# Kernel optimization log

Hardware: AMD Instinct MI355X
Metric: run time of the kernel (lower is better)

Reference implementation:

```python
import jax, jax.numpy as jnp
from jax import lax
import numpy as np

IMG_CH = 3
C = 48            # total channels
HIDDEN = 256
FIRE_RATE = 0.5
DX_NOISE = 0.0
NEG_SLOPE = 0.01  # torch LeakyReLU default


def _dwconv(x_nchw, w):
    # depthwise 3x3 conv with reflect padding, w: [C,1,3,3]
    xp = jnp.pad(x_nchw, ((0, 0), (0, 0), (1, 1), (1, 1)), mode='reflect')
    return lax.conv_general_dilated(
        xp, w, window_strides=(1, 1), padding='VALID',
        feature_group_count=C,
        dimension_numbers=('NCHW', 'OIHW', 'NCHW'))


def setup_inputs() -> dict:
    key = jax.random.key(0)
    ks = jax.random.split(key, 6)
    x = jax.random.normal(ks[0], (8, 256, 256, C), dtype=jnp.float32)
    filt0 = jax.random.normal(ks[1], (C, 1, 3, 3), dtype=jnp.float32) * 0.1
    filt1 = jax.random.normal(ks[2], (C, 1, 3, 3), dtype=jnp.float32) * 0.1
    fan_in = 3 * C
    w1 = jax.random.normal(ks[3], (HIDDEN, 3 * C), dtype=jnp.float32) / np.sqrt(fan_in).astype(np.float32)
    b1 = jax.random.normal(ks[4], (HIDDEN,), dtype=jnp.float32) * 0.01
    # original zero-inits w2; randomized small so outputs/grads are nontrivial
    w2 = jax.random.normal(ks[5], (C, HIDDEN), dtype=jnp.float32) * 0.02
    return {"x": x, "filt0": filt0, "filt1": filt1, "w1": w1, "b1": b1, "w2": w2, "steps": 4}


def reference(x, filt0, filt1, w1, b1, w2, steps):
    ch_mask = (jnp.arange(C) >= IMG_CH).astype(x.dtype)  # immutable image channels
    rng = jax.random.key(42)
    for i in range(steps):
        xc = jnp.transpose(x, (0, 3, 1, 2))                       # [B,C,H,W]
        p = jnp.concatenate([xc, _dwconv(xc, filt0), _dwconv(xc, filt1)], axis=1)
        p = jnp.transpose(p, (0, 2, 3, 1))                        # [B,H,W,3C]
        h = jax.nn.leaky_relu(jnp.einsum('bhwf,of->bhwo', p, w1) + b1, NEG_SLOPE)
        d = jnp.einsum('bhwo,co->bhwc', h, w2)                    # [B,H,W,C]
        k1, k2 = jax.random.split(jax.random.fold_in(rng, i))
        fire = (jax.random.uniform(k1, d.shape[:3] + (1,)) > FIRE_RATE).astype(d.dtype)
        d = d * fire + DX_NOISE * jax.random.normal(k2, d.shape[:3] + (1,), dtype=d.dtype)
        d = d * ch_mask
        x = x + d
    return x
```

## Files before the change

### kernel.cpp

```cpp
#include <hip/hip_runtime.h>
#include <stdint.h>
#include <stddef.h>


#define B_   8
#define H_   256
#define W_   256
#define C_   48
#define F_   144
#define HID_ 256
#define PW_  64
#define NTOT (B_*H_*W_*C_)
#define XSTR 56

typedef __attribute__((ext_vector_type(8))) short short8;
typedef __attribute__((ext_vector_type(4))) float f32x4;

struct U2 { unsigned x, y; };

__host__ __device__ __forceinline__ unsigned rotl32(unsigned v, int r) {
  return (v << r) | (v >> (32 - r));
}

__host__ __device__ __forceinline__ U2 threefry2x32(unsigned k0, unsigned k1,
                                                    unsigned x0, unsigned x1) {
  const unsigned k2 = k0 ^ k1 ^ 0x1BD11BDAu;
  x0 += k0; x1 += k1;
#define TF_R(r) { x0 += x1; x1 = rotl32(x1, r); x1 ^= x0; }
  TF_R(13) TF_R(15) TF_R(26) TF_R(6)
  x0 += k1; x1 += k2 + 1u;
  TF_R(17) TF_R(29) TF_R(16) TF_R(24)
  x0 += k2; x1 += k0 + 2u;
  TF_R(13) TF_R(15) TF_R(26) TF_R(6)
  x0 += k0; x1 += k1 + 3u;
  TF_R(17) TF_R(29) TF_R(16) TF_R(24)
  x0 += k1; x1 += k2 + 4u;
  TF_R(13) TF_R(15) TF_R(26) TF_R(6)
  x0 += k2; x1 += k0 + 5u;
#undef TF_R
  U2 r; r.x = x0; r.y = x1; return r;
}

__device__ __forceinline__ unsigned short f2bf(float f) {
  unsigned u = __float_as_uint(f);
  unsigned r = u + 0x7FFFu + ((u >> 16) & 1u);
  return (unsigned short)(r >> 16);
}
__device__ __forceinline__ unsigned packbf2(float lo, float hi) {
  return (unsigned)f2bf(lo) | ((unsigned)f2bf(hi) << 16);
}
__device__ __forceinline__ float bf2f(unsigned short u) {
  return __uint_as_float(((unsigned)u) << 16);
}

#define W1B_N 114688
#define W2B_N 12288
__global__ void nca_pack(const float* __restrict__ w1,
                         const float* __restrict__ w2,
                         const float* __restrict__ f0,
                         const float* __restrict__ f1,
                         unsigned short* __restrict__ w1B,
                         unsigned short* __restrict__ w2B) {
  int i = blockIdx.x * 256 + threadIdx.x;
  if (i < W1B_N) {
    int ntg = i / 7168, r = i - ntg * 7168;
    int ks = r >> 9, r2 = r & 511;
    int lane = r2 >> 3, j = r2 & 7;
    int o = ntg * 16 + (lane & 15);
    int k = ks * 32 + (lane >> 4) * 8 + j;
    float v = 0.0f;
    if (k < 432) {
      int tap = k / 48, c = k - tap * 48;
      v = w1[o * F_ + 48 + c] * f0[c * 9 + tap]
        + w1[o * F_ + 96 + c] * f1[c * 9 + tap];
      if (tap == 4) v += w1[o * F_ + c];
    }
    w1B[i] = f2bf(v);
  }
  if (i < W2B_N) {
    int nt = i >> 12, r = i & 4095;
    int ks = r >> 9, r2 = r & 511;
    int lane = r2 >> 3, j = r2 & 7;
    int c = nt * 16 + (lane & 15);
    int o = ks * 32 + (lane >> 4) * 8 + j;
    w2B[i] = f2bf(w2[c * HID_ + o]);
  }
}

template<int INBF, int OUTBF>
__global__ __launch_bounds__(256, 3)
void nca_step(const void* __restrict__ xin_, void* __restrict__ xout_,
              const unsigned short* __restrict__ w1B,
              const float* __restrict__ b1,
              const unsigned short* __restrict__ w2Bp,
              unsigned ka, unsigned kb) {
  __shared__ __align__(16) char smem[32768];
  __shared__ float fireL[PW_];
  short* xT = (short*)smem;
  short* hA = (short*)smem;

  const int t = threadIdx.x;
  const int bid = blockIdx.x;
  const int wseg = bid & 3;
  const int h = (bid >> 2) & 255;
  const int b = bid >> 10;
  const int w0 = wseg * PW_;
  const int gbase = ((b * H_ + h) * W_ + w0) * C_;

  if (t < PW_) {
    unsigned j = (unsigned)((b * H_ + h) * W_ + w0 + t);
    U2 r = threefry2x32(ka, kb, 0u, j);
    unsigned bits = r.x ^ r.y;
    fireL[t] = ((bits >> 9) > 4194304u) ? 1.0f : 0.0f;
  }
  {
    const int hr[3] = { (h == 0) ? 1 : h - 1, h, (h == 255) ? 254 : h + 1 };
#pragma unroll
    for (int g = 0; g < 10; ++g) {
      int i = t + g * 256;
      if (i < 2376) {
        int row = i / 792, rem = i - row * 792;
        int px = rem / 12, c4 = rem - px * 12;
        int w = w0 - 1 + px;
        int wg = (w < 0) ? 1 : (w > 255) ? 254 : w;
        const int gidx = ((b * H_ + hr[row]) * W_ + wg) * C_ + c4 * 4;
        uint2 d;
        if constexpr (INBF) {
          d = *(const uint2*)((const unsigned short*)xin_ + gidx);
        } else {
          const float4 v = *(const float4*)((const float*)xin_ + gidx);
          d.x = packbf2(v.x, v.y); d.y = packbf2(v.z, v.w);
        }
        *(uint2*)&xT[(row * 66 + px) * XSTR + c4 * 4] = d;
      }
    }
  }
  __syncthreads();

  const int wv = t >> 6, lane = t & 63;
  const int c16 = lane & 15, quad = lane >> 4;
  f32x4 acc[4][4];
#pragma unroll
  for (int mt = 0; mt < 4; ++mt)
#pragma unroll
    for (int nt = 0; nt < 4; ++nt) acc[mt][nt] = f32x4{0.f, 0.f, 0.f, 0.f};

#define LDA1(dst, ksl) { int ch_ = (ksl) * 4 + quad; \
  if ((ksl) == 13 && ch_ > 53) ch_ = 53;  \
  const int tap_ = ch_ / 6;    \
  const int o_ = ((tap_ / 3) * 66 + c16 + (tap_ - (tap_ / 3) * 3)) * XSTR \
                 + (ch_ - tap_ * 6) * 8; \
  _Pragma("unroll") for (int mt = 0; mt < 4; ++mt) \
    dst[mt] = *(const short8*)&xT[o_ + mt * (16 * XSTR)]; }
#define LDB1(dst, ksl) { _Pragma("unroll") for (int nt = 0; nt < 4; ++nt) \
  dst[nt] = *(const short8*)&w1B[((((wv * 4 + nt) * 14 + (ksl)) << 6) | lane) << 3]; }
#define MM1(aa, bb) { _Pragma("unroll") for (int nt = 0; nt < 4; ++nt) \
  _Pragma("unroll") for (int mt = 0; mt < 4; ++mt) \
    acc[mt][nt] = __builtin_amdgcn_mfma_f32_16x16x32_bf16(aa[mt], bb[nt], acc[mt][nt], 0, 0, 0); }

  {
    short8 aP[4], aQ[4], bX[4], bY[4], bZ[4];
    LDB1(bX, 0) LDB1(bY, 1) LDA1(aP, 0)
    LDA1(aQ, 1)  LDB1(bZ, 2)   MM1(aP, bX)
    LDA1(aP, 2)  LDB1(bX, 3)   MM1(aQ, bY)
    LDA1(aQ, 3)  LDB1(bY, 4)   MM1(aP, bZ)
    LDA1(aP, 4)  LDB1(bZ, 5)   MM1(aQ, bX)
    LDA1(aQ, 5)  LDB1(bX, 6)   MM1(aP, bY)
    LDA1(aP, 6)  LDB1(bY, 7)   MM1(aQ, bZ)
    LDA1(aQ, 7)  LDB1(bZ, 8)   MM1(aP, bX)
    LDA1(aP, 8)  LDB1(bX, 9)   MM1(aQ, bY)
    LDA1(aQ, 9)  LDB1(bY, 10)  MM1(aP, bZ)
    LDA1(aP, 10) LDB1(bZ, 11)  MM1(aQ, bX)
    LDA1(aQ, 11) LDB1(bX, 12)  MM1(aP, bY)
    LDA1(aP, 12) LDB1(bY, 13)  MM1(aQ, bZ)
    LDA1(aQ, 13)               MM1(aP, bX)
                               MM1(aQ, bY)
  }
#undef LDA1
#undef LDB1
#undef MM1

#define LDW2(dst, ksl) { _Pragma("unroll") for (int nt = 0; nt < 3; ++nt) \
  dst[nt] = *(const short8*)&w2Bp[((((nt) * 8 + (ksl)) << 6) | lane) << 3]; }
#define LDH2(dst, ksl) dst = *(const short8*)&hA[(((wv * 8 + (ksl)) << 6) | lane) << 3];
#define MM2(hh, ww) { _Pragma("unroll") for (int nt = 0; nt < 3; ++nt) \
  acc2[nt] = __builtin_amdgcn_mfma_f32_16x16x32_bf16(hh, ww[nt], acc2[nt], 0, 0, 0); }

  short8 wA[3], wB[3], wC[3];
  LDW2(wA, 0) LDW2(wB, 1)

  unsigned short bs[3][4];
  if constexpr (INBF) {
#pragma unroll
    for (int nt = 0; nt < 3; ++nt)
#pragma unroll
      for (int reg = 0; reg < 4; ++reg)
        bs[nt][reg] = (unsigned short)
          xT[(66 + 1 + wv * 16 + quad * 4 + reg) * XSTR + nt * 16 + c16];
  }
  __syncthreads();

#pragma unroll
  for (int nt = 0; nt < 4; ++nt) {
    const int o = (wv * 4 + nt) * 16 + c16;
    const float bias = b1[o];
    const int ks2 = o >> 5, q2 = (o & 31) >> 3, j2 = o & 7;
#pragma unroll
    for (int mt = 0; mt < 4; ++mt) {
#pragma unroll
      for (int reg = 0; reg < 4; ++reg) {
        float z = acc[mt][nt][reg] + bias;
        z = (z >= 0.f) ? z : 0.01f * z;
        const int lane2 = (quad * 4 + reg) + (q2 << 4);
        hA[((((mt * 8 + ks2) << 6) | lane2) << 3) + j2] = (short)f2bf(z);
      }
    }
  }
  __syncthreads();

  {
    f32x4 acc2[3];
#pragma unroll
    for (int nt = 0; nt < 3; ++nt) acc2[nt] = f32x4{0.f, 0.f, 0.f, 0.f};

    short8 h0, h1;
    LDH2(h0, 0)
    LDH2(h1, 1) LDW2(wC, 2) MM2(h0, wA)
    LDH2(h0, 2) LDW2(wA, 3) MM2(h1, wB)
    LDH2(h1, 3) LDW2(wB, 4) MM2(h0, wC)
    LDH2(h0, 4) LDW2(wC, 5) MM2(h1, wA)
    LDH2(h1, 5) LDW2(wA, 6) MM2(h0, wB)
    LDH2(h0, 6) LDW2(wB, 7) MM2(h1, wC)
    LDH2(h1, 7)             MM2(h0, wA)
                            MM2(h1, wB)

#pragma unroll
    for (int nt = 0; nt < 3; ++nt) {
      const int c = nt * 16 + c16;
#pragma unroll
      for (int reg = 0; reg < 4; ++reg) {
        const int pxl = wv * 16 + quad * 4 + reg;
        float d = acc2[nt][reg] * fireL[pxl];
        if (c < 3) d = 0.f;
        const int idx = gbase + pxl * C_ + c;
        float base;
        if constexpr (INBF) base = bf2f(bs[nt][reg]);
        else                base = ((const float*)xin_)[idx];
        const float r = base + d;
        if constexpr (OUTBF) ((unsigned short*)xout_)[idx] = f2bf(r);
        else                 ((float*)xout_)[idx] = r;
      }
    }
  }
#undef LDW2
#undef LDH2
#undef MM2
}

extern "C" void kernel_launch(void* const* d_in, const int* in_sizes, int n_in,
                              void* d_out, int out_size, void* d_ws, size_t ws_size,
                              hipStream_t stream) {
  const float* xin = (const float*)d_in[0];
  const float* f0  = (const float*)d_in[1];
  const float* f1  = (const float*)d_in[2];
  const float* w1  = (const float*)d_in[3];
  const float* b1  = (const float*)d_in[4];
  const float* w2  = (const float*)d_in[5];
  float* xout = (float*)d_out;
  (void)in_sizes; (void)n_in; (void)out_size; (void)ws_size;

  unsigned ka[4], kb[4];
  for (int i = 0; i < 4; ++i) {
    U2 fold = threefry2x32(0u, 42u, 0u, (unsigned)i);
    U2 k1 = threefry2x32(fold.x, fold.y, 0u, 0u);
    ka[i] = k1.x; kb[i] = k1.y;
  }

  unsigned short* w1B = (unsigned short*)d_ws;
  unsigned short* w2B = w1B + W1B_N;
  unsigned short* xb  = (unsigned short*)((char*)d_ws + (size_t)(W1B_N + W2B_N) * 2);
  unsigned short* ob  = (unsigned short*)d_out;

  const dim3 gs(B_ * H_ * (W_ / PW_));
  const dim3 bs(256);

  nca_pack<<<(W1B_N + 255) / 256, 256, 0, stream>>>(w1, w2, f0, f1, w1B, w2B);
  nca_step<0, 1><<<gs, bs, 0, stream>>>(xin, xb,   w1B, b1, w2B, ka[0], kb[0]);
  nca_step<1, 1><<<gs, bs, 0, stream>>>(xb,  ob,   w1B, b1, w2B, ka[1], kb[1]);
  nca_step<1, 1><<<gs, bs, 0, stream>>>(ob,  xb,   w1B, b1, w2B, ka[2], kb[2]);
  nca_step<1, 0><<<gs, bs, 0, stream>>>(xb,  xout, w1B, b1, w2B, ka[3], kb[3]);
}
```

Baseline: 821.6 us.

## Use direct global-to-LDS loads, swap MFMA operands, and pack bf16 conversions

For bf16 inputs, the interior of the halo tile is now loaded straight into LDS with global_load_lds, and the LDS row stride drops from 56 to 48 to match the contiguous layout. Only the edge pixels still go through registers. The w1 packing order changes to k-slice-major, and the MFMA operands are swapped so the accumulator holds output channels along the register dimension. That lets the bias be read as a float4 and the hidden activations stored as packed bf16 pairs using v_cvt_pk_bf16_f32, and the K loop is rewritten as a double-buffered loop. The narrower stride risks LDS bank conflicts, and the hardware rounding may differ slightly from the old software rounding.

```diff
diff --git a/kernel.cpp b/kernel.cpp
--- a/kernel.cpp
+++ b/kernel.cpp
@@ -11,10 +11,16 @@
 #define HID_ 256
 #define PW_  64
 #define NTOT (B_*H_*W_*C_)
-#define XSTR 56
+#define XSTR 48
 
 typedef __attribute__((ext_vector_type(8))) short short8;
 typedef __attribute__((ext_vector_type(4))) float f32x4;
+
+typedef const __attribute__((address_space(1))) char* gas_t;
+typedef __attribute__((address_space(3))) char* las_t;
+__device__ __forceinline__ void gload16(const char* g, char* l) {
+  __builtin_amdgcn_global_load_lds((gas_t)g, (las_t)l, 16, 0, 0);
+}
 
 struct U2 { unsigned x, y; };
 
@@ -41,13 +47,15 @@
   U2 r; r.x = x0; r.y = x1; return r;
 }
 
-__device__ __forceinline__ unsigned short f2bf(float f) {
+__host__ __device__ __forceinline__ unsigned short f2bf(float f) {
   unsigned u = __float_as_uint(f);
   unsigned r = u + 0x7FFFu + ((u >> 16) & 1u);
   return (unsigned short)(r >> 16);
 }
 __device__ __forceinline__ unsigned packbf2(float lo, float hi) {
-  return (unsigned)f2bf(lo) | ((unsigned)f2bf(hi) << 16);
+  unsigned r;
+  asm("v_cvt_pk_bf16_f32 %0, %1, %2" : "=v"(r) : "v"(lo), "v"(hi));
+  return r;
 }
 __device__ __forceinline__ float bf2f(unsigned short u) {
   return __uint_as_float(((unsigned)u) << 16);
@@ -63,8 +71,8 @@
                          unsigned short* __restrict__ w2B) {
   int i = blockIdx.x * 256 + threadIdx.x;
   if (i < W1B_N) {
-    int ntg = i / 7168, r = i - ntg * 7168;
-    int ks = r >> 9, r2 = r & 511;
+    int ks = i >> 13, r = i & 8191;
+    int ntg = r >> 9, r2 = r & 511;
     int lane = r2 >> 3, j = r2 & 7;
     int o = ntg * 16 + (lane & 15);
     int k = ks * 32 + (lane >> 4) * 8 + j;
@@ -115,23 +123,38 @@
   }
   {
     const int hr[3] = { (h == 0) ? 1 : h - 1, h, (h == 255) ? 254 : h + 1 };
-#pragma unroll
-    for (int g = 0; g < 10; ++g) {
-      int i = t + g * 256;
-      if (i < 2376) {
-        int row = i / 792, rem = i - row * 792;
-        int px = rem / 12, c4 = rem - px * 12;
+    if constexpr (INBF) {
+#pragma unroll
+      for (int row = 0; row < 3; ++row) {
+        const char* gs = (const char*)xin_ +
+            (size_t)((b * H_ + hr[row]) * W_ + w0) * (C_ * 2);
+        char* ls = smem + row * (66 * XSTR * 2) + XSTR * 2;
+        gload16(gs + t * 16, ls + t * 16);
+        if (t < 128) gload16(gs + 4096 + t * 16, ls + 4096 + t * 16);
+      }
+      if (t < 72) {
+        int seg = t / 12, u = t - seg * 12;
+        int row = seg >> 1, px = (seg & 1) ? 65 : 0;
         int w = w0 - 1 + px;
         int wg = (w < 0) ? 1 : (w > 255) ? 254 : w;
-        const int gidx = ((b * H_ + hr[row]) * W_ + wg) * C_ + c4 * 4;
-        uint2 d;
-        if constexpr (INBF) {
-          d = *(const uint2*)((const unsigned short*)xin_ + gidx);
-        } else {
+        const int gidx = ((b * H_ + hr[row]) * W_ + wg) * C_ + u * 4;
+        *(uint2*)&xT[(row * 66 + px) * XSTR + u * 4] =
+            *(const uint2*)((const unsigned short*)xin_ + gidx);
+      }
+    } else {
+#pragma unroll
+      for (int g = 0; g < 10; ++g) {
+        int i = t + g * 256;
+        if (i < 2376) {
+          int row = i / 792, rem = i - row * 792;
+          int px = rem / 12, c4 = rem - px * 12;
+          int w = w0 - 1 + px;
+          int wg = (w < 0) ? 1 : (w > 255) ? 254 : w;
+          const int gidx = ((b * H_ + hr[row]) * W_ + wg) * C_ + c4 * 4;
           const float4 v = *(const float4*)((const float*)xin_ + gidx);
-          d.x = packbf2(v.x, v.y); d.y = packbf2(v.z, v.w);
+          uint2 d; d.x = packbf2(v.x, v.y); d.y = packbf2(v.z, v.w);
+          *(uint2*)&xT[(row * 66 + px) * XSTR + c4 * 4] = d;
         }
-        *(uint2*)&xT[(row * 66 + px) * XSTR + c4 * 4] = d;
       }
     }
   }
@@ -141,9 +164,9 @@
   const int c16 = lane & 15, quad = lane >> 4;
   f32x4 acc[4][4];
 #pragma unroll
-  for (int mt = 0; mt < 4; ++mt)
-#pragma unroll
-    for (int nt = 0; nt < 4; ++nt) acc[mt][nt] = f32x4{0.f, 0.f, 0.f, 0.f};
+  for (int i_ = 0; i_ < 4; ++i_)
+#pragma unroll
+    for (int j_ = 0; j_ < 4; ++j_) acc[i_][j_] = f32x4{0.f, 0.f, 0.f, 0.f};
 
 #define LDA1(dst, ksl) { int ch_ = (ksl) * 4 + quad; \
   if ((ksl) == 13 && ch_ > 53) ch_ = 53;  \
@@ -153,28 +176,21 @@
   _Pragma("unroll") for (int mt = 0; mt < 4; ++mt) \
     dst[mt] = *(const short8*)&xT[o_ + mt * (16 * XSTR)]; }
 #define LDB1(dst, ksl) { _Pragma("unroll") for (int nt = 0; nt < 4; ++nt) \
-  dst[nt] = *(const short8*)&w1B[((((wv * 4 + nt) * 14 + (ksl)) << 6) | lane) << 3]; }
+  dst[nt] = *(const short8*)&w1B[((ksl) * 8192) + (wv * 4 + nt) * 512 + lane * 8]; }
 #define MM1(aa, bb) { _Pragma("unroll") for (int nt = 0; nt < 4; ++nt) \
   _Pragma("unroll") for (int mt = 0; mt < 4; ++mt) \
-    acc[mt][nt] = __builtin_amdgcn_mfma_f32_16x16x32_bf16(aa[mt], bb[nt], acc[mt][nt], 0, 0, 0); }
+    acc[nt][mt] = __builtin_amdgcn_mfma_f32_16x16x32_bf16(bb[nt], aa[mt], acc[nt][mt], 0, 0, 0); }
 
   {
-    short8 aP[4], aQ[4], bX[4], bY[4], bZ[4];
-    LDB1(bX, 0) LDB1(bY, 1) LDA1(aP, 0)
-    LDA1(aQ, 1)  LDB1(bZ, 2)   MM1(aP, bX)
-    LDA1(aP, 2)  LDB1(bX, 3)   MM1(aQ, bY)
-    LDA1(aQ, 3)  LDB1(bY, 4)   MM1(aP, bZ)
-    LDA1(aP, 4)  LDB1(bZ, 5)   MM1(aQ, bX)
-    LDA1(aQ, 5)  LDB1(bX, 6)   MM1(aP, bY)
-    LDA1(aP, 6)  LDB1(bY, 7)   MM1(aQ, bZ)
-    LDA1(aQ, 7)  LDB1(bZ, 8)   MM1(aP, bX)
-    LDA1(aP, 8)  LDB1(bX, 9)   MM1(aQ, bY)
-    LDA1(aQ, 9)  LDB1(bY, 10)  MM1(aP, bZ)
-    LDA1(aP, 10) LDB1(bZ, 11)  MM1(aQ, bX)
-    LDA1(aQ, 11) LDB1(bX, 12)  MM1(aP, bY)
-    LDA1(aP, 12) LDB1(bY, 13)  MM1(aQ, bZ)
-    LDA1(aQ, 13)               MM1(aP, bX)
-                               MM1(aQ, bY)
+    short8 aA[4], aB[4], bA[4], bB[4];
+    LDA1(aA, 0) LDB1(bA, 0)
+#pragma unroll
+    for (int kp = 0; kp < 7; ++kp) {
+      LDA1(aB, 2 * kp + 1) LDB1(bB, 2 * kp + 1)
+      MM1(aA, bA)
+      if (kp < 6) { LDA1(aA, 2 * kp + 2) LDB1(bA, 2 * kp + 2) }
+      MM1(aB, bB)
+    }
   }
 #undef LDA1
 #undef LDB1
@@ -201,19 +217,21 @@
   __syncthreads();
 
 #pragma unroll
-  for (int nt = 0; nt < 4; ++nt) {
-    const int o = (wv * 4 + nt) * 16 + c16;
-    const float bias = b1[o];
-    const int ks2 = o >> 5, q2 = (o & 31) >> 3, j2 = o & 7;
-#pragma unroll
-    for (int mt = 0; mt < 4; ++mt) {
-#pragma unroll
-      for (int reg = 0; reg < 4; ++reg) {
-        float z = acc[mt][nt][reg] + bias;
-        z = (z >= 0.f) ? z : 0.01f * z;
-        const int lane2 = (quad * 4 + reg) + (q2 << 4);
-        hA[((((mt * 8 + ks2) << 6) | lane2) << 3) + j2] = (short)f2bf(z);
-      }
+  for (int ont = 0; ont < 4; ++ont) {
+    const int ontg = wv * 4 + ont;
+    const float4 bv = *(const float4*)&b1[ontg * 16 + quad * 4];
+    const int a_ = ontg >> 1, b_ = ontg & 1;
+    const int lp = c16 + 16 * (b_ * 2 + (quad >> 1));
+    const int j0 = (quad & 1) * 4;
+#pragma unroll
+    for (int pxt = 0; pxt < 4; ++pxt) {
+      float z0 = acc[ont][pxt][0] + bv.x; z0 = fmaxf(z0, 0.01f * z0);
+      float z1 = acc[ont][pxt][1] + bv.y; z1 = fmaxf(z1, 0.01f * z1);
+      float z2 = acc[ont][pxt][2] + bv.z; z2 = fmaxf(z2, 0.01f * z2);
+      float z3 = acc[ont][pxt][3] + bv.w; z3 = fmaxf(z3, 0.01f * z3);
+      const int base = (((pxt * 8 + a_) << 6) | lp) << 3;
+      *(unsigned*)&hA[base + j0]     = packbf2(z0, z1);
+      *(unsigned*)&hA[base + j0 + 2] = packbf2(z2, z3);
     }
   }
   __syncthreads();
@@ -237,18 +255,27 @@
 #pragma unroll
     for (int nt = 0; nt < 3; ++nt) {
       const int c = nt * 16 + c16;
+      float r_[4];
 #pragma unroll
       for (int reg = 0; reg < 4; ++reg) {
         const int pxl = wv * 16 + quad * 4 + reg;
         float d = acc2[nt][reg] * fireL[pxl];
         if (c < 3) d = 0.f;
-        const int idx = gbase + pxl * C_ + c;
         float base;
         if constexpr (INBF) base = bf2f(bs[nt][reg]);
-        else                base = ((const float*)xin_)[idx];
-        const float r = base + d;
-        if constexpr (OUTBF) ((unsigned short*)xout_)[idx] = f2bf(r);
-        else                 ((float*)xout_)[idx] = r;
+        else                base = ((const float*)xin_)[gbase + pxl * C_ + c];
+        r_[reg] = base + d;
+        if constexpr (!OUTBF)
+          ((float*)xout_)[gbase + pxl * C_ + c] = r_[reg];
+      }
+      if constexpr (OUTBF) {
+        const unsigned p01 = packbf2(r_[0], r_[1]);
+        const unsigned p23 = packbf2(r_[2], r_[3]);
+        const int i0 = gbase + (wv * 16 + quad * 4) * C_ + c;
+        ((unsigned short*)xout_)[i0]          = (unsigned short)p01;
+        ((unsigned short*)xout_)[i0 + C_]     = (unsigned short)(p01 >> 16);
+        ((unsigned short*)xout_)[i0 + 2 * C_] = (unsigned short)p23;
+        ((unsigned short*)xout_)[i0 + 3 * C_] = (unsigned short)(p23 >> 16);
       }
     }
   }
```

Result: faster. 671.8 us (median of 2 runs) (-18.2%).
